# Optimization experiments

Measured on AMD Instinct MI355X. Metric: run time of the kernel, lower is better.

The kernel has to match this reference:

```python
import jax, jax.numpy as jnp
import numpy as np

D_MODEL, D_K, D_V, NUM_BLOCKS = 1024, 128, 128, 4


def setup_inputs() -> dict:
    key = jax.random.key(0)
    ks = jax.random.split(key, 7)
    B, L = 4, 4096
    s = 1.0 / np.sqrt(D_MODEL)
    return {
        "x": jax.random.normal(ks[0], (B, L, D_MODEL), dtype=jnp.float32),
        "Wq": jax.random.normal(ks[1], (D_K, D_MODEL), dtype=jnp.float32) * s,
        "bq": jnp.zeros((D_K,), dtype=jnp.float32),
        "Wk": jax.random.normal(ks[2], (D_K, D_MODEL), dtype=jnp.float32) * s,
        "bk": jnp.zeros((D_K,), dtype=jnp.float32),
        "Wv": jax.random.normal(ks[3], (D_V, D_MODEL), dtype=jnp.float32) * s,
        "bv": jnp.zeros((D_V,), dtype=jnp.float32),
        "block_idx": 0,
    }


def reference(x, Wq, bq, Wk, bk, Wv, bv, block_idx):
    # Linear projections (torch Linear: y = x W^T + b)
    Q = jnp.einsum("bld,kd->blk", x, Wq) + bq  # [B, L, d_k]
    K = jnp.einsum("bld,kd->blk", x, Wk) + bk  # [B, L, d_k]
    V = jnp.einsum("bld,vd->blv", x, Wv) + bv  # [B, L, d_v]
    scale = 1.0 / np.sqrt(D_K)
    scores = jnp.einsum("blk,bmk->blm", Q, K) * scale  # [B, L, L]
    attn = jax.nn.softmax(scores, axis=-1)
    # The original loops NUM_BLOCKS times over identical K_remote=K, V_remote=V
    # and accumulates; this equals NUM_BLOCKS * (attn @ V).
    output = jnp.float32(NUM_BLOCKS) * jnp.einsum("blm,bmv->blv", attn, V)
    return (output, K, V)
```

## Files before the change

### kernel.cpp

```cpp
#include <hip/hip_runtime.h>

#define B_   4
#define L_   4096
#define DM_  1024
#define DK_  128
#define NSPLIT 4
#define OUT_K_OFF 2097152
#define OUT_V_OFF 4194304

typedef __attribute__((ext_vector_type(4))) float f32x4;
typedef __attribute__((ext_vector_type(8))) short short8;

__device__ __forceinline__ unsigned short f2bf(float f) {
  union { float f; unsigned int u; } v; v.f = f;
  unsigned int u = v.u;
  u += 0x7FFFu + ((u >> 16) & 1u);
  return (unsigned short)(u >> 16);
}
__device__ __forceinline__ float bf2f(unsigned short u) {
  union { unsigned int i; float f; } v; v.i = ((unsigned int)u) << 16; return v.f;
}

#define ASYNC16(gsrc, ldst)                                                          \
  __builtin_amdgcn_global_load_lds(                                                  \
      (const __attribute__((address_space(1))) unsigned int*)(gsrc),                 \
      (__attribute__((address_space(3))) unsigned int*)(ldst), 16, 0, 0)

#define MFMA16(a, b, c) __builtin_amdgcn_mfma_f32_16x16x32_bf16((a), (b), (c), 0, 0, 0)

__global__ __launch_bounds__(256) void cvt_kernel(const float* __restrict__ s,
                                                  unsigned short* __restrict__ d,
                                                  int n8) {
  int i = blockIdx.x * 256 + threadIdx.x;
  if (i >= n8) return;
  const f32x4* p = (const f32x4*)(s + (size_t)i * 8);
  f32x4 a = p[0], b = p[1];
  short8 r;
  r[0] = (short)f2bf(a[0]); r[1] = (short)f2bf(a[1]);
  r[2] = (short)f2bf(a[2]); r[3] = (short)f2bf(a[3]);
  r[4] = (short)f2bf(b[0]); r[5] = (short)f2bf(b[1]);
  r[6] = (short)f2bf(b[2]); r[7] = (short)f2bf(b[3]);
  *(short8*)(d + (size_t)i * 8) = r;
}

__global__ __launch_bounds__(256) void cvtw_kernel(const float* __restrict__ Wq,
                                                   const float* __restrict__ Wk,
                                                   const float* __restrict__ Wv,
                                                   unsigned short* __restrict__ wb) {
  const float* s = (blockIdx.y == 0) ? Wq : (blockIdx.y == 1) ? Wk : Wv;
  unsigned short* d = wb + (size_t)blockIdx.y * (DK_ * DM_);
  int i = blockIdx.x * 256 + threadIdx.x;
  const f32x4* p = (const f32x4*)(s + (size_t)i * 8);
  f32x4 a = p[0], b = p[1];
  short8 r;
  r[0] = (short)f2bf(a[0]); r[1] = (short)f2bf(a[1]);
  r[2] = (short)f2bf(a[2]); r[3] = (short)f2bf(a[3]);
  r[4] = (short)f2bf(b[0]); r[5] = (short)f2bf(b[1]);
  r[6] = (short)f2bf(b[2]); r[7] = (short)f2bf(b[3]);
  *(short8*)(d + (size_t)i * 8) = r;
}

__global__ __launch_bounds__(256) void proj_kernel(
    const unsigned short* __restrict__ xb,
    const unsigned short* __restrict__ wb,
    const float* __restrict__ bias_q, const float* __restrict__ bias_k,
    const float* __restrict__ bias_v,
    unsigned short* __restrict__ qb,
    unsigned short* __restrict__ kb,
    unsigned short* __restrict__ vt,
    float* __restrict__ out) {
  __shared__ __align__(16) char smem[24576];
  char* Alds = smem;
  char* Blds = smem + 8192;

  const int tid  = threadIdx.x;
  const int w    = tid >> 6;
  const int lane = tid & 63;
  const int lo4  = lane & 15, hi4 = lane >> 4;
  const int wm   = w >> 1, wn = w & 1;
  const int mt   = blockIdx.x;
  const int wt   = blockIdx.y;
  const int r0   = mt * 64;
  const unsigned short* wsrc = wb + (size_t)wt * (DK_ * DM_);

  f32x4 acc[2][4];
#pragma unroll
  for (int i = 0; i < 2; i++)
#pragma unroll
    for (int j = 0; j < 4; j++) acc[i][j] = (f32x4){0.f, 0.f, 0.f, 0.f};

  for (int kt = 0; kt < 16; ++kt) {
    const int kc0 = kt * 64;
#pragma unroll
    for (int j = 0; j < 2; ++j) {
      unsigned int o   = (unsigned)(w * 2048 + j * 1024 + lane * 16);
      unsigned int row = o >> 7;
      unsigned int cl  = ((o >> 4) & 7) ^ (row & 7);
      ASYNC16(xb + ((size_t)(r0 + row) * DM_ + kc0 + cl * 8), Alds + w * 2048 + j * 1024);
    }
#pragma unroll
    for (int j = 0; j < 4; ++j) {
      unsigned int o   = (unsigned)(w * 4096 + j * 1024 + lane * 16);
      unsigned int row = o >> 7;
      unsigned int cl  = ((o >> 4) & 7) ^ (row & 7);
      ASYNC16(wsrc + ((size_t)row * DM_ + kc0 + cl * 8), Blds + w * 4096 + j * 1024);
    }
    __syncthreads();
#pragma unroll
    for (int kk = 0; kk < 2; ++kk) {
      short8 af[2], bf[4];
#pragma unroll
      for (int mi = 0; mi < 2; mi++) {
        int row = wm * 32 + mi * 16 + lo4;
        int c   = kk * 4 + hi4;
        af[mi]  = *(const short8*)(Alds + row * 128 + (((c ^ (row & 7))) << 4));
      }
#pragma unroll
      for (int ni = 0; ni < 4; ni++) {
        int col = wn * 64 + ni * 16 + lo4;
        int c   = kk * 4 + hi4;
        bf[ni]  = *(const short8*)(Blds + col * 128 + (((c ^ (col & 7))) << 4));
      }
#pragma unroll
      for (int mi = 0; mi < 2; mi++)
#pragma unroll
        for (int ni = 0; ni < 4; ni++)
          acc[mi][ni] = MFMA16(af[mi], bf[ni], acc[mi][ni]);
    }
    __syncthreads();
  }

  const float* bias = (wt == 0) ? bias_q : (wt == 1) ? bias_k : bias_v;
  float bv4[4];
#pragma unroll
  for (int ni = 0; ni < 4; ni++) bv4[ni] = bias[wn * 64 + ni * 16 + lo4];

  const int b_idx = r0 >> 12;
  const int l0    = r0 & 4095;

  if (wt != 2) {
    unsigned short* dstb = (wt == 0) ? qb : kb;
#pragma unroll
    for (int mi = 0; mi < 2; mi++)
#pragma unroll
      for (int ni = 0; ni < 4; ni++)
#pragma unroll
        for (int reg = 0; reg < 4; reg++) {
          int r   = wm * 32 + mi * 16 + hi4 * 4 + reg;
          int c   = wn * 64 + ni * 16 + lo4;
          float v = acc[mi][ni][reg] + bv4[ni];
          dstb[(size_t)(r0 + r) * DK_ + c] = f2bf(v);
          if (wt == 1) out[OUT_K_OFF + (size_t)(r0 + r) * DK_ + c] = v;
        }
  } else {
    char* T = smem;
#pragma unroll
    for (int mi = 0; mi < 2; mi++)
#pragma unroll
      for (int ni = 0; ni < 4; ni++)
#pragma unroll
        for (int reg = 0; reg < 4; reg++) {
          int r   = wm * 32 + mi * 16 + hi4 * 4 + reg;
          int c   = wn * 64 + ni * 16 + lo4;
          float v = acc[mi][ni][reg] + bv4[ni];
          out[OUT_V_OFF + (size_t)(r0 + r) * DK_ + c] = v;
          *(unsigned short*)(T + c * 144 + r * 2) = f2bf(v);
        }
    __syncthreads();
#pragma unroll
    for (int i = 0; i < 4; ++i) {
      int q = tid + i * 256;
      int d = q >> 3, lg = q & 7;
      short8 s8 = *(const short8*)(T + d * 144 + lg * 16);
      *(short8*)(vt + ((size_t)(b_idx * DK_ + d) * L_ + l0 + lg * 8)) = s8;
    }
  }
}

__global__ __launch_bounds__(256) void attn_kernel(
    const unsigned short* __restrict__ qb, const unsigned short* __restrict__ kb,
    const unsigned short* __restrict__ vt,
    unsigned short* __restrict__ Opart,
    float* __restrict__ ml) {
  __shared__ __align__(16) char smem[40960];
  char* Klds = smem;
  char* Vlds = smem + 16384;

  const int tid  = threadIdx.x;
  const int w    = tid >> 6;
  const int lane = tid & 63;
  const int lo4  = lane & 15, hi4 = lane >> 4;
  char* Plds = smem + 32768 + w * 2048;

  const int qt = blockIdx.x;
  const int b  = blockIdx.y;
  const int sp = blockIdx.z;

  short8 aq[4];
  {
    const unsigned short* qp =
        qb + ((size_t)(b * L_ + qt * 64 + w * 16 + lo4) * DK_ + hi4 * 8);
#pragma unroll
    for (int kc = 0; kc < 4; kc++) aq[kc] = *(const short8*)(qp + kc * 32);
  }

  f32x4 o_acc[8];
#pragma unroll
  for (int dt = 0; dt < 8; dt++) o_acc[dt] = (f32x4){0.f, 0.f, 0.f, 0.f};
  float m[4]  = {-__builtin_inff(), -__builtin_inff(), -__builtin_inff(), -__builtin_inff()};
  float ls[4] = {0.f, 0.f, 0.f, 0.f};
  const float SC = 0.08838834764831845f * 1.4426950408889634f;

  for (int t = sp * 16; t < sp * 16 + 16; ++t) {
#pragma unroll
    for (int j = 0; j < 4; ++j) {
      unsigned int o = (unsigned)(w * 1024 + j * 4096 + lane * 16);
      unsigned int krow = o >> 8;
      unsigned int kcl  = ((o >> 4) & 15) ^ (krow & 7);
      ASYNC16(kb + ((size_t)(b * L_ + t * 64 + krow) * DK_ + kcl * 8),
              Klds + w * 1024 + j * 4096);
      unsigned int d   = o >> 7;
      unsigned int vcl = ((o >> 4) & 7) ^ (d & 7);
      ASYNC16(vt + ((size_t)(b * DK_ + d) * L_ + t * 64 + vcl * 8),
              Vlds + w * 1024 + j * 4096);
    }
    __syncthreads();

    f32x4 s[4];
#pragma unroll
    for (int st = 0; st < 4; st++) s[st] = (f32x4){0.f, 0.f, 0.f, 0.f};
#pragma unroll
    for (int st = 0; st < 4; st++) {
      int key = st * 16 + lo4;
#pragma unroll
      for (int kc = 0; kc < 4; kc++) {
        int c = kc * 4 + hi4;
        short8 bkf = *(const short8*)(Klds + key * 256 + ((c ^ (key & 7)) << 4));
        s[st] = MFMA16(aq[kc], bkf, s[st]);
      }
    }

#pragma unroll
    for (int reg = 0; reg < 4; reg++) {
      float pm = fmaxf(fmaxf(s[0][reg], s[1][reg]), fmaxf(s[2][reg], s[3][reg]));
      pm = fmaxf(pm, __shfl_xor(pm, 1));
      pm = fmaxf(pm, __shfl_xor(pm, 2));
      pm = fmaxf(pm, __shfl_xor(pm, 4));
      pm = fmaxf(pm, __shfl_xor(pm, 8));
      pm *= SC;
      float mn   = fmaxf(m[reg], pm);
      float corr = exp2f(m[reg] - mn);
      m[reg]     = mn;
      float ps   = 0.f;
      int   r    = hi4 * 4 + reg;
#pragma unroll
      for (int st = 0; st < 4; st++) {
        float p = exp2f(s[st][reg] * SC - mn);
        ps += p;
        unsigned int lowb = st * 32 + lo4 * 2;
        unsigned int addr = r * 128 + ((((lowb >> 4) ^ (r & 7)) << 4) | (lowb & 15));
        *(unsigned short*)(Plds + addr) = f2bf(p);
      }
      ls[reg] = ls[reg] * corr + ps;
#pragma unroll
      for (int dt = 0; dt < 8; dt++) o_acc[dt][reg] *= corr;
    }

#pragma unroll
    for (int kk = 0; kk < 2; kk++) {
      int cp = kk * 4 + hi4;
      short8 pa = *(const short8*)(Plds + lo4 * 128 + ((cp ^ (lo4 & 7)) << 4));
#pragma unroll
      for (int dt = 0; dt < 8; dt++) {
        int d = dt * 16 + lo4;
        short8 bvf = *(const short8*)(Vlds + d * 128 + ((cp ^ (d & 7)) << 4));
        o_acc[dt] = MFMA16(pa, bvf, o_acc[dt]);
      }
    }
    __syncthreads();
  }

  float lt[4];
#pragma unroll
  for (int reg = 0; reg < 4; reg++) {
    float t = ls[reg];
    t += __shfl_xor(t, 1);
    t += __shfl_xor(t, 2);
    t += __shfl_xor(t, 4);
    t += __shfl_xor(t, 8);
    lt[reg] = t;
  }
  const size_t rowbase = (size_t)(sp * B_ + b) * L_ + qt * 64 + w * 16;
  if (lo4 == 0) {
#pragma unroll
    for (int reg = 0; reg < 4; reg++) {
      size_t idx = rowbase + hi4 * 4 + reg;
      ml[idx * 2 + 0] = m[reg];
      ml[idx * 2 + 1] = lt[reg];
    }
  }
#pragma unroll
  for (int dt = 0; dt < 8; dt++)
#pragma unroll
    for (int reg = 0; reg < 4; reg++)
      Opart[(rowbase + hi4 * 4 + reg) * 128 + dt * 16 + lo4] = f2bf(o_acc[dt][reg]);
}

__global__ __launch_bounds__(256) void combine_kernel(
    const unsigned short* __restrict__ Opart, const float* __restrict__ ml,
    float* __restrict__ out) {
  const int qt = blockIdx.x, b = blockIdx.y, tid = threadIdx.x;
#pragma unroll
  for (int i = 0; i < 4; ++i) {
    int idx = i * 256 + tid;
    int row = idx >> 4, cg = idx & 15;
    size_t grow = (size_t)b * L_ + qt * 64 + row;
    float ms[NSPLIT], lv[NSPLIT], M = -__builtin_inff();
#pragma unroll
    for (int s = 0; s < NSPLIT; s++) {
      size_t p = ((size_t)s * B_ * L_ + grow) * 2;
      ms[s] = ml[p]; lv[s] = ml[p + 1];
      M = fmaxf(M, ms[s]);
    }
    float acc[8] = {0.f, 0.f, 0.f, 0.f, 0.f, 0.f, 0.f, 0.f};
    float lsum = 0.f;
#pragma unroll
    for (int s = 0; s < NSPLIT; s++) {
      float wgt = exp2f(ms[s] - M);
      lsum += lv[s] * wgt;
      short8 v = *(const short8*)&Opart[((size_t)(s * B_ + b) * L_ + qt * 64 + row) * 128 + cg * 8];
#pragma unroll
      for (int j = 0; j < 8; j++) acc[j] += bf2f((unsigned short)v[j]) * wgt;
    }
    float sc = 4.0f / lsum;
    f32x4 o0 = {acc[0] * sc, acc[1] * sc, acc[2] * sc, acc[3] * sc};
    f32x4 o1 = {acc[4] * sc, acc[5] * sc, acc[6] * sc, acc[7] * sc};
    float* dst = out + grow * 128 + cg * 8;
    *(f32x4*)dst = o0;
    *(f32x4*)(dst + 4) = o1;
  }
}

extern "C" void kernel_launch(void* const* d_in, const int* in_sizes, int n_in,
                              void* d_out, int out_size, void* d_ws, size_t ws_size,
                              hipStream_t stream) {
  const float* x  = (const float*)d_in[0];
  const float* Wq = (const float*)d_in[1];
  const float* bq = (const float*)d_in[2];
  const float* Wk = (const float*)d_in[3];
  const float* bk = (const float*)d_in[4];
  const float* Wv = (const float*)d_in[5];
  const float* bv = (const float*)d_in[6];
  float* out = (float*)d_out;

  unsigned short* xb = (unsigned short*)d_ws;
  unsigned short* wb = xb + (size_t)B_ * L_ * DM_;
  unsigned short* qb = wb + (size_t)3 * DK_ * DM_;
  unsigned short* kb = qb + (size_t)B_ * L_ * DK_;
  unsigned short* vt = kb + (size_t)B_ * L_ * DK_;
  unsigned short* Opart = xb;
  float* ml = (float*)(xb + (size_t)NSPLIT * B_ * L_ * DK_);

  cvt_kernel<<<(B_ * L_ * DM_) / 8 / 256, 256, 0, stream>>>(x, xb, (B_ * L_ * DM_) / 8);
  cvtw_kernel<<<dim3(64, 3), 256, 0, stream>>>(Wq, Wk, Wv, wb);

  proj_kernel<<<dim3(256, 3), 256, 0, stream>>>(xb, wb, bq, bk, bv, qb, kb, vt, out);
  attn_kernel<<<dim3(64, B_, NSPLIT), 256, 0, stream>>>(qb, kb, vt, Opart, ml);
  combine_kernel<<<dim3(64, B_), 256, 0, stream>>>(Opart, ml, out);
}
```

Measured before the change: 228.1 us.

## Double-buffer LDS tiles in projection and attention kernels with async prefetch

New measurement: 234.0 us. +2.6%, slower.

```diff
diff --git a/kernel.cpp b/kernel.cpp
--- a/kernel.cpp
+++ b/kernel.cpp
@@ -1,4 +1,5 @@
 #include <hip/hip_runtime.h>
+#include <hip/hip_bf16.h>
 
 #define B_   4
 #define L_   4096
@@ -12,10 +13,8 @@
 typedef __attribute__((ext_vector_type(8))) short short8;
 
 __device__ __forceinline__ unsigned short f2bf(float f) {
-  union { float f; unsigned int u; } v; v.f = f;
-  unsigned int u = v.u;
-  u += 0x7FFFu + ((u >> 16) & 1u);
-  return (unsigned short)(u >> 16);
+  __hip_bfloat16 h = __float2bfloat16(f);
+  union { __hip_bfloat16 h; unsigned short u; } v; v.h = h; return v.u;
 }
 __device__ __forceinline__ float bf2f(unsigned short u) {
   union { unsigned int i; float f; } v; v.i = ((unsigned int)u) << 16; return v.f;
@@ -27,6 +26,7 @@
       (__attribute__((address_space(3))) unsigned int*)(ldst), 16, 0, 0)
 
 #define MFMA16(a, b, c) __builtin_amdgcn_mfma_f32_16x16x32_bf16((a), (b), (c), 0, 0, 0)
+#define VMCNT0() asm volatile("s_waitcnt vmcnt(0)" ::: "memory")
 
 __global__ __launch_bounds__(256) void cvt_kernel(const float* __restrict__ s,
                                                   unsigned short* __restrict__ d,
@@ -69,9 +69,7 @@
     unsigned short* __restrict__ kb,
     unsigned short* __restrict__ vt,
     float* __restrict__ out) {
-  __shared__ __align__(16) char smem[24576];
-  char* Alds = smem;
-  char* Blds = smem + 8192;
+  __shared__ __align__(16) char smem[49152];
 
   const int tid  = threadIdx.x;
   const int w    = tid >> 6;
@@ -83,29 +81,41 @@
   const int r0   = mt * 64;
   const unsigned short* wsrc = wb + (size_t)wt * (DK_ * DM_);
 
-  f32x4 acc[2][4];
-#pragma unroll
-  for (int i = 0; i < 2; i++)
-#pragma unroll
-    for (int j = 0; j < 4; j++) acc[i][j] = (f32x4){0.f, 0.f, 0.f, 0.f};
-
-  for (int kt = 0; kt < 16; ++kt) {
+  auto stage = [&](int buf, int kt) {
     const int kc0 = kt * 64;
+    char* Al = smem + buf * 24576;
+    char* Bl = Al + 8192;
 #pragma unroll
     for (int j = 0; j < 2; ++j) {
       unsigned int o   = (unsigned)(w * 2048 + j * 1024 + lane * 16);
       unsigned int row = o >> 7;
       unsigned int cl  = ((o >> 4) & 7) ^ (row & 7);
-      ASYNC16(xb + ((size_t)(r0 + row) * DM_ + kc0 + cl * 8), Alds + w * 2048 + j * 1024);
+      ASYNC16(xb + ((size_t)(r0 + row) * DM_ + kc0 + cl * 8), Al + w * 2048 + j * 1024);
     }
 #pragma unroll
     for (int j = 0; j < 4; ++j) {
       unsigned int o   = (unsigned)(w * 4096 + j * 1024 + lane * 16);
       unsigned int row = o >> 7;
       unsigned int cl  = ((o >> 4) & 7) ^ (row & 7);
-      ASYNC16(wsrc + ((size_t)row * DM_ + kc0 + cl * 8), Blds + w * 4096 + j * 1024);
-    }
-    __syncthreads();
+      ASYNC16(wsrc + ((size_t)row * DM_ + kc0 + cl * 8), Bl + w * 4096 + j * 1024);
+    }
+  };
+
+  f32x4 acc[2][4];
+#pragma unroll
+  for (int i = 0; i < 2; i++)
+#pragma unroll
+    for (int j = 0; j < 4; j++) acc[i][j] = (f32x4){0.f, 0.f, 0.f, 0.f};
+
+  stage(0, 0);
+  VMCNT0();
+  __builtin_amdgcn_s_barrier();
+  int cur = 0;
+
+  for (int kt = 0; kt < 16; ++kt) {
+    if (kt < 15) stage(cur ^ 1, kt + 1);
+    char* Alds = smem + cur * 24576;
+    char* Blds = Alds + 8192;
 #pragma unroll
     for (int kk = 0; kk < 2; ++kk) {
       short8 af[2], bf[4];
@@ -127,7 +137,9 @@
         for (int ni = 0; ni < 4; ni++)
           acc[mi][ni] = MFMA16(af[mi], bf[ni], acc[mi][ni]);
     }
-    __syncthreads();
+    VMCNT0();
+    __builtin_amdgcn_s_barrier();
+    cur ^= 1;
   }
 
   const float* bias = (wt == 0) ? bias_q : (wt == 1) ? bias_k : bias_v;
@@ -182,53 +194,65 @@
     const unsigned short* __restrict__ vt,
     unsigned short* __restrict__ Opart,
     float* __restrict__ ml) {
-  __shared__ __align__(16) char smem[40960];
-  char* Klds = smem;
-  char* Vlds = smem + 16384;
+  __shared__ __align__(16) char smem[73728];
 
   const int tid  = threadIdx.x;
   const int w    = tid >> 6;
   const int lane = tid & 63;
   const int lo4  = lane & 15, hi4 = lane >> 4;
-  char* Plds = smem + 32768 + w * 2048;
+  char* Plds = smem + 65536 + w * 2048;
 
   const int qt = blockIdx.x;
   const int b  = blockIdx.y;
   const int sp = blockIdx.z;
-
-  short8 aq[4];
-  {
-    const unsigned short* qp =
-        qb + ((size_t)(b * L_ + qt * 64 + w * 16 + lo4) * DK_ + hi4 * 8);
-#pragma unroll
-    for (int kc = 0; kc < 4; kc++) aq[kc] = *(const short8*)(qp + kc * 32);
-  }
-
-  f32x4 o_acc[8];
-#pragma unroll
-  for (int dt = 0; dt < 8; dt++) o_acc[dt] = (f32x4){0.f, 0.f, 0.f, 0.f};
-  float m[4]  = {-__builtin_inff(), -__builtin_inff(), -__builtin_inff(), -__builtin_inff()};
-  float ls[4] = {0.f, 0.f, 0.f, 0.f};
-  const float SC = 0.08838834764831845f * 1.4426950408889634f;
-
-  for (int t = sp * 16; t < sp * 16 + 16; ++t) {
+  const int t0 = sp * 16;
+
+  auto stage = [&](int buf, int t) {
+    char* Kl = smem + buf * 32768;
+    char* Vl = Kl + 16384;
 #pragma unroll
     for (int j = 0; j < 4; ++j) {
       unsigned int o = (unsigned)(w * 1024 + j * 4096 + lane * 16);
       unsigned int krow = o >> 8;
       unsigned int kcl  = ((o >> 4) & 15) ^ (krow & 7);
       ASYNC16(kb + ((size_t)(b * L_ + t * 64 + krow) * DK_ + kcl * 8),
-              Klds + w * 1024 + j * 4096);
+              Kl + w * 1024 + j * 4096);
       unsigned int d   = o >> 7;
       unsigned int vcl = ((o >> 4) & 7) ^ (d & 7);
       ASYNC16(vt + ((size_t)(b * DK_ + d) * L_ + t * 64 + vcl * 8),
-              Vlds + w * 1024 + j * 4096);
-    }
-    __syncthreads();
+              Vl + w * 1024 + j * 4096);
+    }
+  };
+
+  short8 aq[4];
+  {
+    const unsigned short* qp =
+        qb + ((size_t)(b * L_ + qt * 64 + w * 16 + lo4) * DK_ + hi4 * 8);
+#pragma unroll
+    for (int kc = 0; kc < 4; kc++) aq[kc] = *(const short8*)(qp + kc * 32);
+  }
+
+  f32x4 o_acc[8];
+#pragma unroll
+  for (int dt = 0; dt < 8; dt++) o_acc[dt] = (f32x4){0.f, 0.f, 0.f, 0.f};
+  float m[4]  = {-__builtin_inff(), -__builtin_inff(), -__builtin_inff(), -__builtin_inff()};
+  float ls[4] = {0.f, 0.f, 0.f, 0.f};
+  const float SC = 0.08838834764831845f * 1.4426950408889634f;
+
+  stage(0, t0);
+  VMCNT0();
+  __builtin_amdgcn_s_barrier();
+  int cur = 0;
+
+  for (int i = 0; i < 16; ++i) {
+    if (i < 15) stage(cur ^ 1, t0 + i + 1);
+    char* Klds = smem + cur * 32768;
+    char* Vlds = Klds + 16384;
 
     f32x4 s[4];
 #pragma unroll
     for (int st = 0; st < 4; st++) s[st] = (f32x4){0.f, 0.f, 0.f, 0.f};
+    __builtin_amdgcn_s_setprio(1);
 #pragma unroll
     for (int st = 0; st < 4; st++) {
       int key = st * 16 + lo4;
@@ -239,6 +263,7 @@
         s[st] = MFMA16(aq[kc], bkf, s[st]);
       }
     }
+    __builtin_amdgcn_s_setprio(0);
 
 #pragma unroll
     for (int reg = 0; reg < 4; reg++) {
@@ -248,24 +273,29 @@
       pm = fmaxf(pm, __shfl_xor(pm, 4));
       pm = fmaxf(pm, __shfl_xor(pm, 8));
       pm *= SC;
-      float mn   = fmaxf(m[reg], pm);
-      float corr = exp2f(m[reg] - mn);
-      m[reg]     = mn;
+      if (!__all(pm <= m[reg])) {
+        float mn   = fmaxf(m[reg], pm);
+        float corr = exp2f(m[reg] - mn);
+        m[reg]     = mn;
+        ls[reg]   *= corr;
+#pragma unroll
+        for (int dt = 0; dt < 8; dt++) o_acc[dt][reg] *= corr;
+      }
+      const float mreg = m[reg];
       float ps   = 0.f;
       int   r    = hi4 * 4 + reg;
 #pragma unroll
       for (int st = 0; st < 4; st++) {
-        float p = exp2f(s[st][reg] * SC - mn);
+        float p = exp2f(s[st][reg] * SC - mreg);
         ps += p;
         unsigned int lowb = st * 32 + lo4 * 2;
         unsigned int addr = r * 128 + ((((lowb >> 4) ^ (r & 7)) << 4) | (lowb & 15));
         *(unsigned short*)(Plds + addr) = f2bf(p);
       }
-      ls[reg] = ls[reg] * corr + ps;
-#pragma unroll
-      for (int dt = 0; dt < 8; dt++) o_acc[dt][reg] *= corr;
-    }
-
+      ls[reg] += ps;
+    }
+
+    __builtin_amdgcn_s_setprio(1);
 #pragma unroll
     for (int kk = 0; kk < 2; kk++) {
       int cp = kk * 4 + hi4;
@@ -277,7 +307,11 @@
         o_acc[dt] = MFMA16(pa, bvf, o_acc[dt]);
       }
     }
-    __syncthreads();
+    __builtin_amdgcn_s_setprio(0);
+
+    VMCNT0();
+    __builtin_amdgcn_s_barrier();
+    cur ^= 1;
   }
 
   float lt[4];
```
